# Optimization experiments

Measured on AMD Instinct MI355X. Metric: run time of the kernel, lower is better.

Reference implementation:

```python
import jax, jax.numpy as jnp
import numpy as np

N0, N1, N2 = 16000, 12000, 6000
K0, K1 = 10, 5
H, OUT = 256, 128
VOCABS = [50000, 1000, 200]
EDIMS = [64, 32, 32]
EIN = sum(EDIMS)  # 128 input to fc_input


def setup_inputs() -> dict:
    key = jax.random.key(0)
    ks = jax.random.split(key, 40)
    inp = {}
    cols = [jax.random.randint(ks[i], (N0, 1), 0, VOCABS[i]) for i in range(3)]
    inp['x'] = jnp.concatenate(cols, axis=1)
    inp['idx_sim0'] = jax.random.randint(ks[3], (N1, K0), 0, N0)
    inp['idx_cor0'] = jax.random.randint(ks[4], (N1, K0), 0, N0)
    inp['idx_sim1'] = jax.random.randint(ks[5], (N2, K1), 0, N1)
    inp['idx_cor1'] = jax.random.randint(ks[6], (N2, K1), 0, N1)
    k = 7
    for m in ['sim', 'cor']:
        for i in range(3):
            inp[f'emb{i}_{m}'] = jax.random.normal(ks[k], (VOCABS[i], EDIMS[i]), jnp.float32) * 0.02; k += 1
        inp[f'Win_{m}'] = jax.random.normal(ks[k], (EIN, H), jnp.float32) * (1.0 / np.sqrt(EIN)); k += 1
        inp[f'bin_{m}'] = jnp.zeros((H,), jnp.float32)
        inp[f'Wout_{m}'] = jax.random.normal(ks[k], (H, OUT), jnp.float32) * (1.0 / np.sqrt(H)); k += 1
        inp[f'bout_{m}'] = jnp.zeros((OUT,), jnp.float32)
    inp['Ws2c'] = jax.random.normal(ks[k], (OUT, OUT), jnp.float32) * (1.0 / np.sqrt(OUT)); k += 1
    inp['Wc2s'] = jax.random.normal(ks[k], (OUT, OUT), jnp.float32) * (1.0 / np.sqrt(OUT)); k += 1
    inp['a1'] = jnp.array([0.3], jnp.float32)
    inp['a2'] = jnp.array([0.25], jnp.float32)
    inp['b2'] = jnp.array([0.2], jnp.float32)
    return inp


def _coattention(D, Q):
    # D, Q: [N, K, H]
    L = jnp.einsum('nkh,nmh->nkm', D, Q)          # [N, K, K]
    AC = jax.nn.softmax(L, axis=-1)
    AS = jax.nn.softmax(jnp.swapaxes(L, 1, 2), axis=-1)
    CQ = jnp.einsum('nkm,nmh->nkh', AC, Q)        # [N, K, H]
    CD = jnp.einsum('nkm,nmh->nkh', AS, jnp.concatenate([D, CQ], axis=-1))  # [N, K, 2H]
    return jnp.concatenate([Q, CD], axis=-1)       # [N, K, 3H]


def _coagg(feat, idx_sim, idx_cor, mode, n_dst):
    # gather neighbor features per dst node (feat_src[in_edges_id])
    if mode == 'cor':
        D, Q = feat[idx_sim], feat[idx_cor]
    else:
        D, Q = feat[idx_cor], feat[idx_sim]
    h = _coattention(D, Q)                         # [n_dst, K, 3H]
    n, k, f = h.shape
    # AvgPool1d(kernel=3, stride=3) over feature axis -> [n_dst, K, H]
    pooled = h.reshape(n, k, f // 3, 3).mean(axis=-1)
    neigh = pooled.mean(axis=1)                    # mean over neighbors -> [n_dst, H]
    return feat[:n_dst] + neigh


def _branch(x, e0, e1, e2, Win, bin_, Wout, bout, i_s0, i_c0, i_s1, i_c1, mode):
    e = jnp.concatenate([e0[x[:, 0]], e1[x[:, 1]], e2[x[:, 2]]], axis=1)  # [N0, 128]
    h = e @ Win + bin_                             # [N0, H]
    h = jax.nn.relu(_coagg(h, i_s0, i_c0, mode, N1))
    h = _coagg(h, i_s1, i_c1, mode, N2)
    return h @ Wout + bout                         # [N2, OUT]


def reference(x, idx_sim0, idx_cor0, idx_sim1, idx_cor1,
              emb0_sim, emb1_sim, emb2_sim, Win_sim, bin_sim, Wout_sim, bout_sim,
              emb0_cor, emb1_cor, emb2_cor, Win_cor, bin_cor, Wout_cor, bout_cor,
              Ws2c, Wc2s, a1, a2, b2):
    sim = _branch(x, emb0_sim, emb1_sim, emb2_sim, Win_sim, bin_sim, Wout_sim, bout_sim,
                  idx_sim0, idx_cor0, idx_sim1, idx_cor1, 'sim')
    cor = _branch(x, emb0_cor, emb1_cor, emb2_cor, Win_cor, bin_cor, Wout_cor, bout_cor,
                  idx_sim0, idx_cor0, idx_sim1, idx_cor1, 'cor')
    # SemanticIntegration
    z1sim = (1 - a1) * sim + a1 * (cor @ Wc2s)
    z1cor = (1 - a1) * cor + a1 * (sim @ Ws2c)
    z2sim = (1 - a2 - b2) * sim + a2 * (cor @ Wc2s) + b2 * (z1cor @ Wc2s)
    z2cor = (1 - a2 - b2) * cor + a2 * (sim @ Ws2c) + b2 * (z1sim @ Ws2c)
    return jnp.stack([z2sim, z2cor])               # [2, N2, OUT]
```

## Files before the change

kernel.cpp:

```cpp
#include <hip/hip_runtime.h>

#define CH 256

template <int CTRL>
__device__ __forceinline__ float dppAdd(float v) {
    const int m = __builtin_amdgcn_update_dpp(0, __builtin_bit_cast(int, v), CTRL, 0xf, 0xf, true);
    return v + __builtin_bit_cast(float, m);
}

#define OPAQUE4(v) asm volatile("" : "+v"((v).x), "+v"((v).y), "+v"((v).z), "+v"((v).w))

__global__ __launch_bounds__(256) void embed_fc2_kernel(
    const int* __restrict__ x,
    const float* __restrict__ e0a, const float* __restrict__ e1a, const float* __restrict__ e2a,
    const float* __restrict__ Wina, const float* __restrict__ bina, float* __restrict__ h0a,
    const float* __restrict__ e0b, const float* __restrict__ e1b, const float* __restrict__ e2b,
    const float* __restrict__ Winb, const float* __restrict__ binb, float* __restrict__ h0b,
    const int blocksPer)
{
    __shared__ __align__(16) float eT[128][32];
    int bid = blockIdx.x;
    const float *e0, *e1, *e2, *Win, *bin;
    float* h0;
    if (bid < blocksPer) { e0 = e0a; e1 = e1a; e2 = e2a; Win = Wina; bin = bina; h0 = h0a; }
    else { bid -= blocksPer; e0 = e0b; e1 = e1b; e2 = e2b; Win = Winb; bin = binb; h0 = h0b; }

    const int row0 = bid * 32;
    const int t = threadIdx.x;
    const int w = t >> 6, l = t & 63;
    const int r = l & 31;
    const int kcBase = 2 * w + (l >> 5);

#pragma unroll
    for (int j = 0; j < 4; ++j) {
        const int kc = kcBase + 8 * j;
        const int k0 = kc * 4;
        const int row = row0 + r;
        float4 v;
        if (kc < 16)      v = *(const float4*)(e0 + (size_t)x[row * 3 + 0] * 64 + k0);
        else if (kc < 24) v = *(const float4*)(e1 + (size_t)x[row * 3 + 1] * 32 + (k0 - 64));
        else              v = *(const float4*)(e2 + (size_t)x[row * 3 + 2] * 32 + (k0 - 96));
        eT[k0 + 0][r] = v.x; eT[k0 + 1][r] = v.y; eT[k0 + 2][r] = v.z; eT[k0 + 3][r] = v.w;
    }
    __syncthreads();

    const float4 bb = *(const float4*)(bin + l * 4);
    float acc[8][4];
#pragma unroll
    for (int rr = 0; rr < 8; ++rr) {
        acc[rr][0] = bb.x; acc[rr][1] = bb.y; acc[rr][2] = bb.z; acc[rr][3] = bb.w;
    }
#pragma unroll 4
    for (int k = 0; k < 128; ++k) {
        const float4 wv = *(const float4*)(Win + (size_t)k * 256 + l * 4);
        const float4 ea = *(const float4*)&eT[k][w * 8];
        const float4 eb = *(const float4*)&eT[k][w * 8 + 4];
        const float ev[8] = {ea.x, ea.y, ea.z, ea.w, eb.x, eb.y, eb.z, eb.w};
#pragma unroll
        for (int rr = 0; rr < 8; ++rr) {
            acc[rr][0] += ev[rr] * wv.x; acc[rr][1] += ev[rr] * wv.y;
            acc[rr][2] += ev[rr] * wv.z; acc[rr][3] += ev[rr] * wv.w;
        }
    }
#pragma unroll
    for (int rr = 0; rr < 8; ++rr) {
        float4 o = make_float4(acc[rr][0], acc[rr][1], acc[rr][2], acc[rr][3]);
        *(float4*)(h0 + (size_t)(row0 + w * 8 + rr) * 256 + l * 4) = o;
    }
}

template <int KD, int MODE>
__global__ __launch_bounds__(256) void gemm32_kernel(
    const float* __restrict__ ina, const float* __restrict__ Wa,
    const float* __restrict__ auxa, const float* __restrict__ aux2a, float* __restrict__ oa,
    const float* __restrict__ inb, const float* __restrict__ Wb,
    const float* __restrict__ auxb, const float* __restrict__ aux2b, float* __restrict__ ob,
    const int blocksPer, const int nRows,
    const float* __restrict__ a1p, const float* __restrict__ a2p, const float* __restrict__ b2p)
{
    __shared__ __align__(16) float inT[KD][32];
    int bid = blockIdx.x;
    const float *in, *W, *aux, *aux2; float* outp;
    if (bid < blocksPer) { in = ina; W = Wa; aux = auxa; aux2 = aux2a; outp = oa; }
    else { bid -= blocksPer; in = inb; W = Wb; aux = auxb; aux2 = aux2b; outp = ob; }

    const int row0 = bid * 32;
    const int t = threadIdx.x;
    const int w = t >> 6, l = t & 63;
    const int r = l & 31;
    const int kcBase = 2 * w + (l >> 5);

#pragma unroll
    for (int j = 0; j < KD / 32; ++j) {
        const int kc = kcBase + 8 * j;
        const int k0 = kc * 4;
        int row = row0 + r;
        if (row >= nRows) row = nRows - 1;
        const float4 v = *(const float4*)(in + (size_t)row * KD + k0);
        inT[k0 + 0][r] = v.x; inT[k0 + 1][r] = v.y; inT[k0 + 2][r] = v.z; inT[k0 + 3][r] = v.w;
    }
    __syncthreads();

    const int rg = w * 2 + (l >> 5);
    const int r0 = rg * 4;
    const int cc0 = (l & 31) * 4;

    float acc[4][4];
    if constexpr (MODE == 0) {
        const float4 bb = *(const float4*)(aux + cc0);
#pragma unroll
        for (int rr = 0; rr < 4; ++rr) {
            acc[rr][0] = bb.x; acc[rr][1] = bb.y; acc[rr][2] = bb.z; acc[rr][3] = bb.w;
        }
    } else {
#pragma unroll
        for (int rr = 0; rr < 4; ++rr) acc[rr][0] = acc[rr][1] = acc[rr][2] = acc[rr][3] = 0.f;
    }

#pragma unroll 4
    for (int k = 0; k < KD; ++k) {
        const float4 wv = *(const float4*)(W + (size_t)k * 128 + cc0);
        const float4 ea = *(const float4*)&inT[k][r0];
        const float ev[4] = {ea.x, ea.y, ea.z, ea.w};
#pragma unroll
        for (int rr = 0; rr < 4; ++rr) {
            acc[rr][0] += ev[rr] * wv.x; acc[rr][1] += ev[rr] * wv.y;
            acc[rr][2] += ev[rr] * wv.z; acc[rr][3] += ev[rr] * wv.w;
        }
    }

    float c0 = 0.f, c1 = 0.f, c2 = 0.f;
    if constexpr (MODE == 1) {
        const float a1 = *a1p, a2 = *a2p, b2 = *b2p;
        c0 = 1.f - a2 - b2;
        c1 = a2 + b2 * (1.f - a1);
        c2 = b2 * a1;
    }

#pragma unroll
    for (int rr = 0; rr < 4; ++rr) {
        const int row = row0 + r0 + rr;
        if (row < nRows) {
            float4 o = make_float4(acc[rr][0], acc[rr][1], acc[rr][2], acc[rr][3]);
            if constexpr (MODE == 1) {
                const size_t idx = (size_t)row * 128 + cc0;
                const float4 b1v = *(const float4*)(aux + idx);
                const float4 b2v = *(const float4*)(aux2 + idx);
                o.x = c0 * b1v.x + c1 * b2v.x + c2 * o.x;
                o.y = c0 * b1v.y + c1 * b2v.y + c2 * o.y;
                o.z = c0 * b1v.z + c1 * b2v.z + c2 * o.z;
                o.w = c0 * b1v.w + c1 * b2v.w + c2 * o.w;
            }
            *(float4*)(outp + (size_t)row * 128 + cc0) = o;
        }
    }
}

template <int K>
__global__ __launch_bounds__(256, 2) void coagg_kernel(
    const float* __restrict__ fa, const int* __restrict__ iDa, const int* __restrict__ iQa,
    float* __restrict__ oa,
    const float* __restrict__ fb, const int* __restrict__ iDb, const int* __restrict__ iQb,
    float* __restrict__ ob,
    const int nPer, const int relu)
{
    __shared__ float sL[4][K][K];
    __shared__ float sLT[4][K][K];
    __shared__ float sAC[4][K][K];
    __shared__ float sAS[4][K][K];
    __shared__ float sw_[4][K], su_[4][K];
    __shared__ __align__(16) float sHsum[4][768];

    const int t = threadIdx.x;
    const int wv = t >> 6, lane = t & 63;
    int n = blockIdx.x * 4 + wv;

    const float* feat; const int* idxD; const int* idxQ; float* outp;
    if (n < nPer) { feat = fa; idxD = iDa; idxQ = iQa; outp = oa; }
    else { n -= nPer; feat = fb; idxD = iDb; idxQ = iQb; outp = ob; }

    const float4* fp = (const float4*)feat;

    float4 d[K], q[K];
#pragma unroll
    for (int k = 0; k < K; ++k) {
        const int rD = idxD[n * K + k];
        const int rQ = idxQ[n * K + k];
        d[k] = fp[(size_t)rD * 64 + lane];
        q[k] = fp[(size_t)rQ * 64 + lane];
    }
    const float4 resid = fp[(size_t)n * 64 + lane];
#pragma unroll
    for (int k = 0; k < K; ++k) { OPAQUE4(d[k]); OPAQUE4(q[k]); }

#pragma unroll
    for (int k = 0; k < K; ++k) {
        const float4 dd = d[k];
#pragma unroll
        for (int m0 = 0; m0 < K; m0 += 2) {
            const float4 q0 = q[m0];
            float s0 = dd.x * q0.x + dd.y * q0.y + dd.z * q0.z + dd.w * q0.w;
            float s1 = 0.f;
            if (m0 + 1 < K) {
                const float4 q1 = q[m0 + 1];
                s1 = dd.x * q1.x + dd.y * q1.y + dd.z * q1.z + dd.w * q1.w;
            }
            asm volatile("v_permlane32_swap_b32 %0, %1" : "+v"(s0), "+v"(s1));
            float r = s0 + s1;
            r = dppAdd<0x111>(r);
            r = dppAdd<0x112>(r);
            r = dppAdd<0x114>(r);
            r = dppAdd<0x118>(r);
            r = dppAdd<0x142>(r);
            if (lane == 31) { sL[wv][k][m0] = r; sLT[wv][m0][k] = r; }
            if (lane == 63 && m0 + 1 < K) { sL[wv][k][m0 + 1] = r; sLT[wv][m0 + 1][k] = r; }
        }
    }

    {
        const int g = lane >> 4;
        const int r2 = lane & 15;
        if (g < 2 && r2 < K) {
            const float* Lrow = (g == 0) ? &sL[wv][r2][0] : &sLT[wv][r2][0];
            float* Arow       = (g == 0) ? &sAC[wv][r2][0] : &sAS[wv][r2][0];
            float e_[K], mx = -1e30f;
#pragma unroll
            for (int m = 0; m < K; ++m) mx = fmaxf(mx, Lrow[m]);
            float ssum = 0.f;
#pragma unroll
            for (int m = 0; m < K; ++m) { e_[m] = __expf(Lrow[m] - mx); ssum += e_[m]; }
            const float inv = 1.f / ssum;
#pragma unroll
            for (int m = 0; m < K; ++m) Arow[m] = e_[m] * inv;
        }
    }
    {
        const int m2 = lane - 32;
        if (m2 >= 0 && m2 < K) {
            float s = 0.f;
#pragma unroll
            for (int k2 = 0; k2 < K; ++k2) s += sAS[wv][k2][m2];
            sw_[wv][m2] = s;
        }
    }
    {
        const int j2 = lane - 48;
        if (j2 >= 0 && j2 < K) {
            float s = 0.f;
#pragma unroll
            for (int m = 0; m < K; ++m) s += sw_[wv][m] * sAC[wv][m][j2];
            su_[wv][j2] = s;
        }
    }

    float4 h0v = make_float4(0.f, 0.f, 0.f, 0.f);
    float4 h1v = make_float4(0.f, 0.f, 0.f, 0.f);
    float4 h2v = make_float4(0.f, 0.f, 0.f, 0.f);
#pragma unroll
    for (int kx = 0; kx < K; ++kx) {
        const float wk = sw_[wv][kx];
        const float uk = su_[wv][kx];
        const float4 qq = q[kx];
        const float4 dd = d[kx];
        h0v.x += qq.x;      h0v.y += qq.y;      h0v.z += qq.z;      h0v.w += qq.w;
        h1v.x += wk * dd.x; h1v.y += wk * dd.y; h1v.z += wk * dd.z; h1v.w += wk * dd.w;
        h2v.x += uk * qq.x; h2v.y += uk * qq.y; h2v.z += uk * qq.z; h2v.w += uk * qq.w;
    }
    ((float4*)&sHsum[wv][0])[lane]       = h0v;
    ((float4*)&sHsum[wv][0])[64 + lane]  = h1v;
    ((float4*)&sHsum[wv][0])[128 + lane] = h2v;

    float ov[4];
#pragma unroll
    for (int i = 0; i < 4; ++i) {
        const int f = lane * 4 + i;
        ov[i] = (sHsum[wv][3 * f] + sHsum[wv][3 * f + 1] + sHsum[wv][3 * f + 2])
                * (1.0f / (3.0f * K));
    }
    float4 o = make_float4(resid.x + ov[0], resid.y + ov[1],
                           resid.z + ov[2], resid.w + ov[3]);
    if (relu) {
        o.x = fmaxf(o.x, 0.f); o.y = fmaxf(o.y, 0.f);
        o.z = fmaxf(o.z, 0.f); o.w = fmaxf(o.w, 0.f);
    }
    ((float4*)outp)[(size_t)n * 64 + lane] = o;
}

extern "C" void kernel_launch(void* const* d_in, const int* in_sizes, int n_in,
                              void* d_out, int out_size, void* d_ws, size_t ws_size,
                              hipStream_t stream)
{
    const int* x        = (const int*)d_in[0];
    const int* idx_sim0 = (const int*)d_in[1];
    const int* idx_cor0 = (const int*)d_in[2];
    const int* idx_sim1 = (const int*)d_in[3];
    const int* idx_cor1 = (const int*)d_in[4];
    const float* e0s  = (const float*)d_in[5];
    const float* e1s  = (const float*)d_in[6];
    const float* e2s  = (const float*)d_in[7];
    const float* Wins = (const float*)d_in[8];
    const float* bins = (const float*)d_in[9];
    const float* Wouts= (const float*)d_in[10];
    const float* bouts= (const float*)d_in[11];
    const float* e0c  = (const float*)d_in[12];
    const float* e1c  = (const float*)d_in[13];
    const float* e2c  = (const float*)d_in[14];
    const float* Winc = (const float*)d_in[15];
    const float* binc = (const float*)d_in[16];
    const float* Woutc= (const float*)d_in[17];
    const float* boutc= (const float*)d_in[18];
    const float* Ws2c = (const float*)d_in[19];
    const float* Wc2s = (const float*)d_in[20];
    const float* a1 = (const float*)d_in[21];
    const float* a2 = (const float*)d_in[22];
    const float* b2 = (const float*)d_in[23];

    float* outSim = (float*)d_out;
    float* outCor = outSim + 6000 * 128;

    float* ws = (float*)d_ws;
    const size_t needMerged = (size_t)(2 * 16000 * 256 + 2 * 12000 * 256 + 2 * 6000 * 256 + 4 * 6000 * 128) * 4;
    const bool merged = ws_size >= needMerged;

    const int fcBlocks = (6000 + 31) / 32;

    if (merged) {
        float* A0 = ws;
        float* A1 = A0 + 16000 * 256;
        float* B0 = A1 + 16000 * 256;
        float* B1 = B0 + 12000 * 256;
        float* C0 = B1 + 12000 * 256;
        float* C1 = C0 + 6000 * 256;
        float* simO = C1 + 6000 * 256;
        float* corO = simO + 6000 * 128;
        float* P    = corO + 6000 * 128;
        float* S    = P + 6000 * 128;

        embed_fc2_kernel<<<1000, 256, 0, stream>>>(x,
            e0s, e1s, e2s, Wins, bins, A0,
            e0c, e1c, e2c, Winc, binc, A1, 500);
        coagg_kernel<10><<<6000, 256, 0, stream>>>(
            A0, idx_cor0, idx_sim0, B0,
            A1, idx_sim0, idx_cor0, B1, 12000, 1);
        coagg_kernel<5><<<3000, 256, 0, stream>>>(
            B0, idx_cor1, idx_sim1, C0,
            B1, idx_sim1, idx_cor1, C1, 6000, 0);
        gemm32_kernel<256, 0><<<2 * fcBlocks, 256, 0, stream>>>(
            C0, Wouts, bouts, nullptr, simO,
            C1, Woutc, boutc, nullptr, corO, fcBlocks, 6000, a1, a2, b2);
        gemm32_kernel<128, 2><<<2 * fcBlocks, 256, 0, stream>>>(
            corO, Wc2s, nullptr, nullptr, P,
            simO, Ws2c, nullptr, nullptr, S, fcBlocks, 6000, a1, a2, b2);
        gemm32_kernel<128, 1><<<2 * fcBlocks, 256, 0, stream>>>(
            S, Wc2s, simO, P, outSim,
            P, Ws2c, corO, S, outCor, fcBlocks, 6000, a1, a2, b2);
    } else {
        float* A = ws;
        float* B = A + 16000 * 256;
        float* C = B + 12000 * 256;
        float* simO = C + 6000 * 256;
        float* corO = simO + 6000 * 128;
        float* P    = corO + 6000 * 128;
        float* S    = P + 6000 * 128;

        for (int b = 0; b < 2; ++b) {
            const float* e0   = (b == 0) ? e0s : e0c;
            const float* e1   = (b == 0) ? e1s : e1c;
            const float* e2   = (b == 0) ? e2s : e2c;
            const float* Win  = (b == 0) ? Wins : Winc;
            const float* bin  = (b == 0) ? bins : binc;
            const float* Wout = (b == 0) ? Wouts : Woutc;
            const float* bout = (b == 0) ? bouts : boutc;
            const int* iD0 = (b == 0) ? idx_cor0 : idx_sim0;
            const int* iQ0 = (b == 0) ? idx_sim0 : idx_cor0;
            const int* iD1 = (b == 0) ? idx_cor1 : idx_sim1;
            const int* iQ1 = (b == 0) ? idx_sim1 : idx_cor1;
            float* branchOut = (b == 0) ? simO : corO;

            embed_fc2_kernel<<<500, 256, 0, stream>>>(x,
                e0, e1, e2, Win, bin, A,
                e0, e1, e2, Win, bin, A, 500);
            coagg_kernel<10><<<3000, 256, 0, stream>>>(
                A, iD0, iQ0, B, A, iD0, iQ0, B, 12000, 1);
            coagg_kernel<5><<<1500, 256, 0, stream>>>(
                B, iD1, iQ1, C, B, iD1, iQ1, C, 6000, 0);
            gemm32_kernel<256, 0><<<fcBlocks, 256, 0, stream>>>(
                C, Wout, bout, nullptr, branchOut,
                C, Wout, bout, nullptr, branchOut, fcBlocks, 6000, a1, a2, b2);
        }
        gemm32_kernel<128, 2><<<2 * fcBlocks, 256, 0, stream>>>(
            corO, Wc2s, nullptr, nullptr, P,
            simO, Ws2c, nullptr, nullptr, S, fcBlocks, 6000, a1, a2, b2);
        gemm32_kernel<128, 1><<<2 * fcBlocks, 256, 0, stream>>>(
            S, Wc2s, simO, P, outSim,
            P, Ws2c, corO, S, outCor, fcBlocks, 6000, a1, a2, b2);
    }
}
```

Measured before the change: 182.5 us.

## Fuse output projection and semantic integration GEMMs into one tail kernel

Replaces the three tail GEMM launches (Wout projection, cross projections, final mix) with a single kernel that keeps the sim/cor rows and intermediate S/P products in shared memory. The final combination is rewritten algebraically into three coefficients applied to sim, first cross product, and second cross product. This removes two launches and global writes/reads of intermediates, at the cost of smaller 16-row tiles that reread the weight matrices per block.

```diff
diff --git a/kernel.cpp b/kernel.cpp
--- a/kernel.cpp
+++ b/kernel.cpp
@@ -66,6 +66,143 @@
     for (int rr = 0; rr < 8; ++rr) {
         float4 o = make_float4(acc[rr][0], acc[rr][1], acc[rr][2], acc[rr][3]);
         *(float4*)(h0 + (size_t)(row0 + w * 8 + rr) * 256 + l * 4) = o;
+    }
+}
+
+__global__ __launch_bounds__(256) void tail_fused_kernel(
+    const float* __restrict__ C0, const float* __restrict__ C1,
+    const float* __restrict__ Wouts, const float* __restrict__ bouts,
+    const float* __restrict__ Woutc, const float* __restrict__ boutc,
+    const float* __restrict__ Ws2c, const float* __restrict__ Wc2s,
+    const float* __restrict__ a1p, const float* __restrict__ a2p,
+    const float* __restrict__ b2p,
+    float* __restrict__ outSim, float* __restrict__ outCor)
+{
+    __shared__ __align__(16) float c0T[256][16];
+    __shared__ __align__(16) float c1T[256][16];
+    __shared__ float xT0[128][17];
+    __shared__ float xT1[128][17];
+
+    const int t = threadIdx.x;
+    const int w = t >> 6, l = t & 63;
+    const int row0 = blockIdx.x * 16;
+
+    {
+        const int row = t >> 4;
+        const int kc  = t & 15;
+        const float4* s0 = (const float4*)(C0 + (size_t)(row0 + row) * 256);
+        const float4* s1 = (const float4*)(C1 + (size_t)(row0 + row) * 256);
+#pragma unroll
+        for (int j = 0; j < 4; ++j) {
+            const int kq = kc + 16 * j;
+            const int k0 = 4 * kq;
+            float4 v = s0[kq];
+            c0T[k0 + 0][row] = v.x; c0T[k0 + 1][row] = v.y;
+            c0T[k0 + 2][row] = v.z; c0T[k0 + 3][row] = v.w;
+            v = s1[kq];
+            c1T[k0 + 0][row] = v.x; c1T[k0 + 1][row] = v.y;
+            c1T[k0 + 2][row] = v.z; c1T[k0 + 3][row] = v.w;
+        }
+    }
+    __syncthreads();
+
+    const int r0 = w * 4;
+    const int cc = l * 2;
+
+    float sim[4][2], cor[4][2];
+    {
+        const float2 bs = *(const float2*)(bouts + cc);
+        const float2 bc = *(const float2*)(boutc + cc);
+#pragma unroll
+        for (int rr = 0; rr < 4; ++rr) {
+            sim[rr][0] = bs.x; sim[rr][1] = bs.y;
+            cor[rr][0] = bc.x; cor[rr][1] = bc.y;
+        }
+    }
+#pragma unroll 4
+    for (int k = 0; k < 256; ++k) {
+        const float4 a0 = *(const float4*)&c0T[k][r0];
+        const float4 a1v = *(const float4*)&c1T[k][r0];
+        const float2 wsv = *(const float2*)(Wouts + (size_t)k * 128 + cc);
+        const float2 wcv = *(const float2*)(Woutc + (size_t)k * 128 + cc);
+        const float e0[4] = {a0.x, a0.y, a0.z, a0.w};
+        const float e1[4] = {a1v.x, a1v.y, a1v.z, a1v.w};
+#pragma unroll
+        for (int rr = 0; rr < 4; ++rr) {
+            sim[rr][0] += e0[rr] * wsv.x; sim[rr][1] += e0[rr] * wsv.y;
+            cor[rr][0] += e1[rr] * wcv.x; cor[rr][1] += e1[rr] * wcv.y;
+        }
+    }
+#pragma unroll
+    for (int rr = 0; rr < 4; ++rr) {
+        xT0[cc + 0][r0 + rr] = sim[rr][0]; xT0[cc + 1][r0 + rr] = sim[rr][1];
+        xT1[cc + 0][r0 + rr] = cor[rr][0]; xT1[cc + 1][r0 + rr] = cor[rr][1];
+    }
+    __syncthreads();
+
+    float S[4][2], P[4][2];
+#pragma unroll
+    for (int rr = 0; rr < 4; ++rr) S[rr][0] = S[rr][1] = P[rr][0] = P[rr][1] = 0.f;
+#pragma unroll 4
+    for (int k = 0; k < 128; ++k) {
+        const float s0 = xT0[k][r0 + 0], s1 = xT0[k][r0 + 1],
+                    s2 = xT0[k][r0 + 2], s3 = xT0[k][r0 + 3];
+        const float p0 = xT1[k][r0 + 0], p1 = xT1[k][r0 + 1],
+                    p2 = xT1[k][r0 + 2], p3 = xT1[k][r0 + 3];
+        const float2 wS = *(const float2*)(Ws2c + (size_t)k * 128 + cc);
+        const float2 wC = *(const float2*)(Wc2s + (size_t)k * 128 + cc);
+        S[0][0] += s0 * wS.x; S[0][1] += s0 * wS.y;
+        S[1][0] += s1 * wS.x; S[1][1] += s1 * wS.y;
+        S[2][0] += s2 * wS.x; S[2][1] += s2 * wS.y;
+        S[3][0] += s3 * wS.x; S[3][1] += s3 * wS.y;
+        P[0][0] += p0 * wC.x; P[0][1] += p0 * wC.y;
+        P[1][0] += p1 * wC.x; P[1][1] += p1 * wC.y;
+        P[2][0] += p2 * wC.x; P[2][1] += p2 * wC.y;
+        P[3][0] += p3 * wC.x; P[3][1] += p3 * wC.y;
+    }
+    __syncthreads();
+#pragma unroll
+    for (int rr = 0; rr < 4; ++rr) {
+        xT0[cc + 0][r0 + rr] = S[rr][0]; xT0[cc + 1][r0 + rr] = S[rr][1];
+        xT1[cc + 0][r0 + rr] = P[rr][0]; xT1[cc + 1][r0 + rr] = P[rr][1];
+    }
+    __syncthreads();
+
+    float T1[4][2], T2[4][2];
+#pragma unroll
+    for (int rr = 0; rr < 4; ++rr) T1[rr][0] = T1[rr][1] = T2[rr][0] = T2[rr][1] = 0.f;
+#pragma unroll 4
+    for (int k = 0; k < 128; ++k) {
+        const float s0 = xT0[k][r0 + 0], s1 = xT0[k][r0 + 1],
+                    s2 = xT0[k][r0 + 2], s3 = xT0[k][r0 + 3];
+        const float p0 = xT1[k][r0 + 0], p1 = xT1[k][r0 + 1],
+                    p2 = xT1[k][r0 + 2], p3 = xT1[k][r0 + 3];
+        const float2 wC = *(const float2*)(Wc2s + (size_t)k * 128 + cc);
+        const float2 wS = *(const float2*)(Ws2c + (size_t)k * 128 + cc);
+        T1[0][0] += s0 * wC.x; T1[0][1] += s0 * wC.y;
+        T1[1][0] += s1 * wC.x; T1[1][1] += s1 * wC.y;
+        T1[2][0] += s2 * wC.x; T1[2][1] += s2 * wC.y;
+        T1[3][0] += s3 * wC.x; T1[3][1] += s3 * wC.y;
+        T2[0][0] += p0 * wS.x; T2[0][1] += p0 * wS.y;
+        T2[1][0] += p1 * wS.x; T2[1][1] += p1 * wS.y;
+        T2[2][0] += p2 * wS.x; T2[2][1] += p2 * wS.y;
+        T2[3][0] += p3 * wS.x; T2[3][1] += p3 * wS.y;
+    }
+
+    const float a1 = *a1p, a2 = *a2p, b2 = *b2p;
+    const float k0 = 1.f - a2 - b2;
+    const float k1 = a2 + b2 * (1.f - a1);
+    const float k2 = b2 * a1;
+#pragma unroll
+    for (int rr = 0; rr < 4; ++rr) {
+        const size_t idx = (size_t)(row0 + r0 + rr) * 128 + cc;
+        float2 oS, oC;
+        oS.x = k0 * sim[rr][0] + k1 * P[rr][0] + k2 * T1[rr][0];
+        oS.y = k0 * sim[rr][1] + k1 * P[rr][1] + k2 * T1[rr][1];
+        oC.x = k0 * cor[rr][0] + k1 * S[rr][0] + k2 * T2[rr][0];
+        oC.y = k0 * cor[rr][1] + k1 * S[rr][1] + k2 * T2[rr][1];
+        *(float2*)(outSim + idx) = oS;
+        *(float2*)(outCor + idx) = oC;
     }
 }
 
@@ -331,10 +468,6 @@
         float* B1 = B0 + 12000 * 256;
         float* C0 = B1 + 12000 * 256;
         float* C1 = C0 + 6000 * 256;
-        float* simO = C1 + 6000 * 256;
-        float* corO = simO + 6000 * 128;
-        float* P    = corO + 6000 * 128;
-        float* S    = P + 6000 * 128;
 
         embed_fc2_kernel<<<1000, 256, 0, stream>>>(x,
             e0s, e1s, e2s, Wins, bins, A0,
@@ -345,15 +478,9 @@
         coagg_kernel<5><<<3000, 256, 0, stream>>>(
             B0, idx_cor1, idx_sim1, C0,
             B1, idx_sim1, idx_cor1, C1, 6000, 0);
-        gemm32_kernel<256, 0><<<2 * fcBlocks, 256, 0, stream>>>(
-            C0, Wouts, bouts, nullptr, simO,
-            C1, Woutc, boutc, nullptr, corO, fcBlocks, 6000, a1, a2, b2);
-        gemm32_kernel<128, 2><<<2 * fcBlocks, 256, 0, stream>>>(
-            corO, Wc2s, nullptr, nullptr, P,
-            simO, Ws2c, nullptr, nullptr, S, fcBlocks, 6000, a1, a2, b2);
-        gemm32_kernel<128, 1><<<2 * fcBlocks, 256, 0, stream>>>(
-            S, Wc2s, simO, P, outSim,
-            P, Ws2c, corO, S, outCor, fcBlocks, 6000, a1, a2, b2);
+        tail_fused_kernel<<<375, 256, 0, stream>>>(
+            C0, C1, Wouts, bouts, Woutc, boutc, Ws2c, Wc2s,
+            a1, a2, b2, outSim, outCor);
     } else {
         float* A = ws;
         float* B = A + 16000 * 256;
```

Measured after the change: 192.7 us. 1.06x slower.
